# Kernel optimization log

Hardware: AMD Instinct MI355X
Metric: run time of the kernel (lower is better)

## Reference

```python
import jax, jax.numpy as jnp
import numpy as np


def _quat_to_rot(q):
    # q: (N,4) wxyz -> (N,3,3)
    q = q / jnp.linalg.norm(q, axis=1, keepdims=True)
    w, x, y, z = q[:, 0], q[:, 1], q[:, 2], q[:, 3]
    R = jnp.stack([
        1 - 2 * y * y - 2 * z * z, 2 * x * y - 2 * w * z, 2 * x * z + 2 * w * y,
        2 * x * y + 2 * w * z, 1 - 2 * x * x - 2 * z * z, 2 * y * z - 2 * w * x,
        2 * x * z - 2 * w * y, 2 * y * z + 2 * w * x, 1 - 2 * x * x - 2 * y * y,
    ], axis=1)
    return R.reshape(-1, 3, 3)


def _forward(camera_poses, positions, scales, rotations, opacity, features, H, W):
    B = camera_poses.shape[0]
    N = positions.shape[0]
    # --- project positions: hom @ pose^T ---
    hom = jnp.concatenate([positions, jnp.ones((N, 1), positions.dtype)], axis=1)  # (N,4)
    cam = jnp.einsum('ni,bji->bnj', hom, camera_poses)  # (B,N,4)
    depths = cam[..., 2]                                 # (B,N)
    pos2d = cam[..., :2] / depths[..., None]             # (B,N,2)
    # --- 3D covariance: R S S R^T ---
    R = _quat_to_rot(rotations)                          # (N,3,3)
    cov3d = jnp.einsum('nik,nk,njk->nij', R, scales * scales, R)  # (N,3,3)
    # --- perspective Jacobian (original uses world-space z, kept faithful) ---
    fx = camera_poses[:, 0, 0][:, None]  # (B,1)
    fy = camera_poses[:, 1, 1][:, None]
    z = positions[:, 2][None, :]         # (1,N)
    zero = jnp.zeros_like(fx * z)        # (B,N)
    row0 = jnp.stack([fx / z, zero, -fx * positions[None, :, 0] / (z * z)], axis=-1)
    row1 = jnp.stack([zero, fy / z, -fy * positions[None, :, 1] / (z * z)], axis=-1)
    J = jnp.stack([row0, row1], axis=-2)                 # (B,N,2,3)
    cov2d = jnp.einsum('bnij,njk,bnlk->bnil', J, cov3d, J)  # (B,N,2,2)
    # --- back-to-front order (descending depth) ---
    order = jnp.argsort(-depths, axis=1)                 # (B,N)
    pos_s = jnp.take_along_axis(pos2d, order[..., None], axis=1)
    cov_s = jnp.take_along_axis(cov2d, order[..., None, None], axis=1)
    color_s = features[order]                            # (B,N,3)
    alpha_s = opacity[order, 0]                          # (B,N)
    # analytic 2x2 inverse
    a = cov_s[..., 0, 0]; b = cov_s[..., 0, 1]; c = cov_s[..., 1, 0]; d = cov_s[..., 1, 1]
    det = a * d - b * c
    inv = jnp.stack([jnp.stack([d, -b], -1), jnp.stack([-c, a], -1)], -2) / det[..., None, None]
    # pixel grid in [-1,1], (H,W,2) with x first (matches torch stack([x,y]))
    ys = jnp.linspace(-1.0, 1.0, H)
    xs = jnp.linspace(-1.0, 1.0, W)
    yy, xx = jnp.meshgrid(ys, xs, indexing='ij')
    grid = jnp.stack([xx, yy], axis=-1)
    # --- splat + alpha compositing (sequential loop expressed as exclusive cumprod) ---
    diff = grid[None, None] - pos_s[:, :, None, None, :]           # (B,N,H,W,2)
    maha = jnp.einsum('bnhwi,bnij,bnhwj->bnhw', diff, inv, diff)   # (B,N,H,W)
    alpha_map = jnp.exp(-0.5 * maha) * alpha_s[:, :, None, None]   # (B,N,H,W)
    trans = jnp.cumprod(1.0 - alpha_map, axis=1)
    T = jnp.concatenate([jnp.ones_like(trans[:, :1]), trans[:, :-1]], axis=1)  # exclusive
    weight = T * alpha_map
    return jnp.einsum('bnhw,bnc->bchw', weight, color_s)          # (B,3,H,W)


def setup_inputs() -> dict:
    key = jax.random.key(0)
    ks = jax.random.split(key, 6)
    N, B = 2048, 1
    positions = jax.random.uniform(ks[0], (N, 3), minval=-1.0, maxval=1.0)
    scales = jax.random.uniform(ks[1], (N, 3), minval=0.001, maxval=0.1)
    rot = jnp.concatenate([jnp.ones((N, 1)), 0.01 * jax.random.normal(ks[2], (N, 3))], axis=1)
    rotations = rot / jnp.linalg.norm(rot, axis=1, keepdims=True)
    opacity = jax.random.uniform(ks[3], (N, 1), minval=0.0, maxval=0.02)
    features = jax.random.uniform(ks[4], (N, 3))
    pose = jnp.eye(4) + 0.01 * jax.random.normal(ks[5], (4, 4))
    pose = pose.at[2, 3].add(3.0).at[3].set(jnp.array([0.0, 0.0, 0.0, 1.0]))
    camera_poses = jnp.broadcast_to(pose, (B, 4, 4))
    return {"camera_poses": camera_poses, "positions": positions, "scales": scales,
            "rotations": rotations, "opacity": opacity, "features": features,
            "H": 96, "W": 96}


def reference(camera_poses, positions, scales, rotations, opacity, features, H, W):
    return _forward(camera_poses, positions, scales, rotations, opacity, features, H, W)
```

## Files before the change

kernel.cpp:

```cpp
#include <hip/hip_runtime.h>
#include <math.h>

#define TPB 256
#define PIXPT 4
#define NSEG_MAX 64

__device__ __forceinline__ unsigned int f2ord(float f) {
    unsigned int u = __float_as_uint(f);
    return (u & 0x80000000u) ? ~u : (u | 0x80000000u);
}

__global__ void gs_preprocess(const float* __restrict__ pose,
                              const float* __restrict__ positions,
                              const float* __restrict__ scales,
                              const float* __restrict__ rotations,
                              const float* __restrict__ opacity,
                              const float* __restrict__ features,
                              float* __restrict__ params,
                              unsigned long long* __restrict__ keys,
                              int N, int B)
{
    int idx = blockIdx.x * blockDim.x + threadIdx.x;
    if (idx >= B * N) return;
    int b = idx / N;
    int n = idx - b * N;
    const float* P = pose + b * 16;
    const float C_EXP = -0.72134752044448170f;

    float x = positions[n * 3 + 0];
    float y = positions[n * 3 + 1];
    float z = positions[n * 3 + 2];

    float depth = P[8] * x + P[9] * y + P[10] * z + P[11];
    float inv_d = 1.0f / depth;
    float mx = (P[0] * x + P[1] * y + P[2] * z + P[3]) * inv_d;
    float my = (P[4] * x + P[5] * y + P[6] * z + P[7]) * inv_d;

    float qw = rotations[n * 4 + 0];
    float qx = rotations[n * 4 + 1];
    float qy = rotations[n * 4 + 2];
    float qz = rotations[n * 4 + 3];
    float qn = sqrtf(qw * qw + qx * qx + qy * qy + qz * qz);
    qw /= qn; qx /= qn; qy /= qn; qz /= qn;
    float R00 = 1.f - 2.f * (qy * qy + qz * qz);
    float R01 = 2.f * (qx * qy - qw * qz);
    float R02 = 2.f * (qx * qz + qw * qy);
    float R10 = 2.f * (qx * qy + qw * qz);
    float R11 = 1.f - 2.f * (qx * qx + qz * qz);
    float R12 = 2.f * (qy * qz - qw * qx);
    float R20 = 2.f * (qx * qz - qw * qy);
    float R21 = 2.f * (qy * qz + qw * qx);
    float R22 = 1.f - 2.f * (qx * qx + qy * qy);

    float s0 = scales[n * 3 + 0];
    float s1 = scales[n * 3 + 1];
    float s2 = scales[n * 3 + 2];
    float v0 = s0 * s0, v1 = s1 * s1, v2 = s2 * s2;

    float C00 = R00 * R00 * v0 + R01 * R01 * v1 + R02 * R02 * v2;
    float C01 = R00 * R10 * v0 + R01 * R11 * v1 + R02 * R12 * v2;
    float C02 = R00 * R20 * v0 + R01 * R21 * v1 + R02 * R22 * v2;
    float C11 = R10 * R10 * v0 + R11 * R11 * v1 + R12 * R12 * v2;
    float C12 = R10 * R20 * v0 + R11 * R21 * v1 + R12 * R22 * v2;
    float C22 = R20 * R20 * v0 + R21 * R21 * v1 + R22 * R22 * v2;

    float fx = P[0], fy = P[5];
    float iz = 1.0f / z;
    float a0 = fx * iz;
    float c0 = -fx * x * iz * iz;
    float b1 = fy * iz;
    float c1 = -fy * y * iz * iz;

    float cov00 = a0 * a0 * C00 + 2.f * a0 * c0 * C02 + c0 * c0 * C22;
    float cov01 = a0 * b1 * C01 + a0 * c1 * C02 + c0 * b1 * C12 + c0 * c1 * C22;
    float cov11 = b1 * b1 * C11 + 2.f * b1 * c1 * C12 + c1 * c1 * C22;

    float det = cov00 * cov11 - cov01 * cov01;
    float invdet = 1.0f / det;
    float A  = C_EXP * cov11 * invdet;
    float Bc = C_EXP * -2.0f * cov01 * invdet;
    float D  = C_EXP * cov00 * invdet;
    float l2a = log2f(opacity[n]);

    float4* p4 = (float4*)(params + (size_t)idx * 12);
    p4[0] = make_float4(mx, my, A, Bc);
    p4[1] = make_float4(D, l2a, features[n * 3 + 0], features[n * 3 + 1]);
    p4[2] = make_float4(features[n * 3 + 2], 0.f, 0.f, 0.f);

    keys[idx] = ((unsigned long long)(~f2ord(depth)) << 32) | (unsigned int)n;
}

__global__ void gs_rank(const unsigned long long* __restrict__ keys,
                        int* __restrict__ order,
                        int N)
{
    extern __shared__ unsigned long long skey[];
    int b = blockIdx.y;
    const unsigned long long* kb = keys + (size_t)b * N;
    for (int i = threadIdx.x; i < N; i += blockDim.x) skey[i] = kb[i];
    __syncthreads();

    int g = blockIdx.x * 32 + (threadIdx.x >> 3);
    int s = threadIdx.x & 7;
    if (g >= N) return;
    unsigned long long kn = skey[g];
    int chunk = (N + 7) >> 3;
    int m0 = s * chunk;
    int m1 = m0 + chunk; if (m1 > N) m1 = N;
    int cnt = 0;
    #pragma unroll 4
    for (int m = m0; m < m1; ++m) cnt += (skey[m] < kn) ? 1 : 0;
    cnt += __shfl_down(cnt, 4, 8);
    cnt += __shfl_down(cnt, 2, 8);
    cnt += __shfl_down(cnt, 1, 8);
    if (s == 0) order[(size_t)b * N + cnt] = g;
}

__global__ void gs_raster_partial(const float* __restrict__ params,
                                  const int* __restrict__ order,
                                  float* __restrict__ partials,
                                  const int* __restrict__ pH,
                                  const int* __restrict__ pW,
                                  int N, int B, int HW, int nseg)
{
    extern __shared__ float4 sg4[];
    int H = *pH;
    int W = *pW;
    int seg = blockIdx.y;
    int seglen = (N + nseg - 1) / nseg;
    int g0 = seg * seglen;
    int g1 = g0 + seglen; if (g1 > N) g1 = N;
    int cnt = g1 - g0; if (cnt < 0) cnt = 0;

    int pixbase = blockIdx.x * (TPB * PIXPT);
    int b = pixbase / HW;

    const int* ob = order + (size_t)b * N + g0;
    for (int i = threadIdx.x; i < cnt * 3; i += TPB) {
        int gi = i / 3;
        int r  = i - gi * 3;
        int idx = ob[gi];
        sg4[i] = ((const float4*)(params + ((size_t)b * N + idx) * 12))[r];
    }
    __syncthreads();

    float px[PIXPT], py[PIXPT];
    float T[PIXPT], cr[PIXPT], cg[PIXPT], cb[PIXPT];
    bool valid[PIXPT];
    #pragma unroll
    for (int k = 0; k < PIXPT; ++k) {
        int pix = pixbase + threadIdx.x + k * TPB;
        valid[k] = (pix < B * HW);
        int pp = valid[k] ? (pix - b * HW) : 0;
        int h = pp / W;
        int w = pp - h * W;
        px[k] = 2.0f * (float)w / (float)(W - 1) - 1.0f;
        py[k] = 2.0f * (float)h / (float)(H - 1) - 1.0f;
        T[k] = 1.0f; cr[k] = 0.f; cg[k] = 0.f; cb[k] = 0.f;
    }

    for (int g = 0; g < cnt; ++g) {
        float4 f0 = sg4[g * 3 + 0];
        float4 f1 = sg4[g * 3 + 1];
        float4 f2 = sg4[g * 3 + 2];
        #pragma unroll
        for (int k = 0; k < PIXPT; ++k) {
            float dx = px[k] - f0.x;
            float dy = py[k] - f0.y;
            float q = f1.y;
            q = fmaf(f1.x * dy, dy, q);
            q = fmaf(f0.w * dx, dy, q);
            q = fmaf(f0.z * dx, dx, q);
            float am = exp2f(q);
            float wgt = T[k] * am;
            cr[k] = fmaf(wgt, f1.z, cr[k]);
            cg[k] = fmaf(wgt, f1.w, cg[k]);
            cb[k] = fmaf(wgt, f2.x, cb[k]);
            T[k] = fmaf(-am, T[k], T[k]);
        }
    }

    #pragma unroll
    for (int k = 0; k < PIXPT; ++k) {
        int pix = pixbase + threadIdx.x + k * TPB;
        if (!valid[k]) continue;
        float4* o = (float4*)(partials + ((size_t)seg * (size_t)(B * HW) + pix) * 4);
        *o = make_float4(cr[k], cg[k], cb[k], T[k]);
    }
}

__global__ void gs_combine(const float* __restrict__ partials,
                           float* __restrict__ out,
                           int B, int HW, int nseg)
{
    int pix = blockIdx.x * blockDim.x + threadIdx.x;
    if (pix >= B * HW) return;
    int b = pix / HW;
    int pp = pix - b * HW;
    float T = 1.0f, cr = 0.f, cg = 0.f, cb = 0.f;
    for (int s = 0; s < nseg; ++s) {
        float4 p = *(const float4*)(partials + ((size_t)s * (size_t)(B * HW) + pix) * 4);
        cr = fmaf(T, p.x, cr);
        cg = fmaf(T, p.y, cg);
        cb = fmaf(T, p.z, cb);
        T *= p.w;
    }
    out[((size_t)b * 3 + 0) * HW + pp] = cr;
    out[((size_t)b * 3 + 1) * HW + pp] = cg;
    out[((size_t)b * 3 + 2) * HW + pp] = cb;
}

extern "C" void kernel_launch(void* const* d_in, const int* in_sizes, int n_in,
                              void* d_out, int out_size, void* d_ws, size_t ws_size,
                              hipStream_t stream)
{
    const float* pose      = (const float*)d_in[0];
    const float* positions = (const float*)d_in[1];
    const float* scales    = (const float*)d_in[2];
    const float* rotations = (const float*)d_in[3];
    const float* opacity   = (const float*)d_in[4];
    const float* features  = (const float*)d_in[5];
    const int*   pH        = (const int*)d_in[6];
    const int*   pW        = (const int*)d_in[7];

    int B = in_sizes[0] / 16;
    int N = in_sizes[1] / 3;
    int HW = out_size / (3 * B);

    float* out = (float*)d_out;

    char* wp = (char*)d_ws;
    float* params = (float*)wp;
    wp += ((size_t)B * N * 12 * sizeof(float) + 15) & ~(size_t)15;
    unsigned long long* keys = (unsigned long long*)wp;
    wp += ((size_t)B * N * sizeof(unsigned long long) + 15) & ~(size_t)15;
    int* order = (int*)wp;
    wp += ((size_t)B * N * sizeof(int) + 15) & ~(size_t)15;
    float* partials = (float*)wp;

    size_t used = (size_t)(wp - (char*)d_ws);
    size_t avail = ws_size > used ? ws_size - used : 0;
    long long ns = (long long)(avail / ((size_t)B * HW * 4 * sizeof(float)));
    int nseg = (int)(ns > NSEG_MAX ? NSEG_MAX : ns);
    if (nseg < 1) nseg = 1;

    int bn = B * N;
    gs_preprocess<<<(bn + TPB - 1) / TPB, TPB, 0, stream>>>(
        pose, positions, scales, rotations, opacity, features,
        params, keys, N, B);

    dim3 g2((N + 31) / 32, B);
    gs_rank<<<g2, TPB, N * sizeof(unsigned long long), stream>>>(keys, order, N);

    int seglen = (N + nseg - 1) / nseg;
    dim3 g3((B * HW + TPB * PIXPT - 1) / (TPB * PIXPT), nseg);
    gs_raster_partial<<<g3, TPB, (size_t)seglen * 3 * sizeof(float4), stream>>>(
        params, order, partials, pH, pW, N, B, HW, nseg);

    gs_combine<<<(B * HW + TPB - 1) / TPB, TPB, 0, stream>>>(
        partials, out, B, HW, nseg);
}
```

Before: 124.3 us.

## Fuse preprocess and rank kernels, scatter params directly in sorted order

Merges the preprocessing and rank-counting kernels into one launch. Each block recomputes all depth keys into shared memory, ranks its Gaussians, and the rank-0 lane of each group computes the full parameters and writes them straight to their sorted slot. The raster kernel then reads the sorted parameter array contiguously instead of gathering through an order index. This removes one launch, the keys and order buffers, and the indirect gather. In exchange, every block recomputes all N depths, and the per-Gaussian math runs on only one lane in eight, which is divergent. The rank loop now uses a strided access pattern instead of contiguous chunks.

Result: faster. 120.9 us (-2.8%).

```diff
diff --git a/kernel.cpp b/kernel.cpp
--- a/kernel.cpp
+++ b/kernel.cpp
@@ -10,36 +10,54 @@
     return (u & 0x80000000u) ? ~u : (u | 0x80000000u);
 }
 
-__global__ void gs_preprocess(const float* __restrict__ pose,
-                              const float* __restrict__ positions,
-                              const float* __restrict__ scales,
-                              const float* __restrict__ rotations,
-                              const float* __restrict__ opacity,
-                              const float* __restrict__ features,
-                              float* __restrict__ params,
-                              unsigned long long* __restrict__ keys,
-                              int N, int B)
-{
-    int idx = blockIdx.x * blockDim.x + threadIdx.x;
-    if (idx >= B * N) return;
-    int b = idx / N;
-    int n = idx - b * N;
+__global__ void gs_prep_rank(const float* __restrict__ pose,
+                             const float* __restrict__ positions,
+                             const float* __restrict__ scales,
+                             const float* __restrict__ rotations,
+                             const float* __restrict__ opacity,
+                             const float* __restrict__ features,
+                             float* __restrict__ sorted,
+                             int N)
+{
+    extern __shared__ unsigned long long skey[];
+    const int b = blockIdx.y;
     const float* P = pose + b * 16;
     const float C_EXP = -0.72134752044448170f;
 
-    float x = positions[n * 3 + 0];
-    float y = positions[n * 3 + 1];
-    float z = positions[n * 3 + 2];
+    for (int n = threadIdx.x; n < N; n += TPB) {
+        float x = positions[n * 3 + 0];
+        float y = positions[n * 3 + 1];
+        float z = positions[n * 3 + 2];
+        float depth = P[8] * x + P[9] * y + P[10] * z + P[11];
+        skey[n] = ((unsigned long long)(~f2ord(depth)) << 32) | (unsigned int)n;
+    }
+    __syncthreads();
+
+    int g = blockIdx.x * 32 + (threadIdx.x >> 3);
+    int s = threadIdx.x & 7;
+    if (g >= N) return;
+    unsigned long long kn = skey[g];
+    int cnt = 0;
+    for (int m = s; m < N; m += 8) cnt += (skey[m] < kn) ? 1 : 0;
+    cnt += __shfl_down(cnt, 4, 8);
+    cnt += __shfl_down(cnt, 2, 8);
+    cnt += __shfl_down(cnt, 1, 8);
+    if (s != 0) return;
+    int rank = cnt;
+
+    float x = positions[g * 3 + 0];
+    float y = positions[g * 3 + 1];
+    float z = positions[g * 3 + 2];
 
     float depth = P[8] * x + P[9] * y + P[10] * z + P[11];
     float inv_d = 1.0f / depth;
     float mx = (P[0] * x + P[1] * y + P[2] * z + P[3]) * inv_d;
     float my = (P[4] * x + P[5] * y + P[6] * z + P[7]) * inv_d;
 
-    float qw = rotations[n * 4 + 0];
-    float qx = rotations[n * 4 + 1];
-    float qy = rotations[n * 4 + 2];
-    float qz = rotations[n * 4 + 3];
+    float qw = rotations[g * 4 + 0];
+    float qx = rotations[g * 4 + 1];
+    float qy = rotations[g * 4 + 2];
+    float qz = rotations[g * 4 + 3];
     float qn = sqrtf(qw * qw + qx * qx + qy * qy + qz * qz);
     qw /= qn; qx /= qn; qy /= qn; qz /= qn;
     float R00 = 1.f - 2.f * (qy * qy + qz * qz);
@@ -52,9 +70,9 @@
     float R21 = 2.f * (qy * qz + qw * qx);
     float R22 = 1.f - 2.f * (qx * qx + qy * qy);
 
-    float s0 = scales[n * 3 + 0];
-    float s1 = scales[n * 3 + 1];
-    float s2 = scales[n * 3 + 2];
+    float s0 = scales[g * 3 + 0];
+    float s1 = scales[g * 3 + 1];
+    float s2 = scales[g * 3 + 2];
     float v0 = s0 * s0, v1 = s1 * s1, v2 = s2 * s2;
 
     float C00 = R00 * R00 * v0 + R01 * R01 * v1 + R02 * R02 * v2;
@@ -80,44 +98,15 @@
     float A  = C_EXP * cov11 * invdet;
     float Bc = C_EXP * -2.0f * cov01 * invdet;
     float D  = C_EXP * cov00 * invdet;
-    float l2a = log2f(opacity[n]);
-
-    float4* p4 = (float4*)(params + (size_t)idx * 12);
+    float l2a = log2f(opacity[g]);
+
+    float4* p4 = (float4*)(sorted + ((size_t)b * N + rank) * 12);
     p4[0] = make_float4(mx, my, A, Bc);
-    p4[1] = make_float4(D, l2a, features[n * 3 + 0], features[n * 3 + 1]);
-    p4[2] = make_float4(features[n * 3 + 2], 0.f, 0.f, 0.f);
-
-    keys[idx] = ((unsigned long long)(~f2ord(depth)) << 32) | (unsigned int)n;
-}
-
-__global__ void gs_rank(const unsigned long long* __restrict__ keys,
-                        int* __restrict__ order,
-                        int N)
-{
-    extern __shared__ unsigned long long skey[];
-    int b = blockIdx.y;
-    const unsigned long long* kb = keys + (size_t)b * N;
-    for (int i = threadIdx.x; i < N; i += blockDim.x) skey[i] = kb[i];
-    __syncthreads();
-
-    int g = blockIdx.x * 32 + (threadIdx.x >> 3);
-    int s = threadIdx.x & 7;
-    if (g >= N) return;
-    unsigned long long kn = skey[g];
-    int chunk = (N + 7) >> 3;
-    int m0 = s * chunk;
-    int m1 = m0 + chunk; if (m1 > N) m1 = N;
-    int cnt = 0;
-    #pragma unroll 4
-    for (int m = m0; m < m1; ++m) cnt += (skey[m] < kn) ? 1 : 0;
-    cnt += __shfl_down(cnt, 4, 8);
-    cnt += __shfl_down(cnt, 2, 8);
-    cnt += __shfl_down(cnt, 1, 8);
-    if (s == 0) order[(size_t)b * N + cnt] = g;
-}
-
-__global__ void gs_raster_partial(const float* __restrict__ params,
-                                  const int* __restrict__ order,
+    p4[1] = make_float4(D, l2a, features[g * 3 + 0], features[g * 3 + 1]);
+    p4[2] = make_float4(features[g * 3 + 2], 0.f, 0.f, 0.f);
+}
+
+__global__ void gs_raster_partial(const float* __restrict__ sorted,
                                   float* __restrict__ partials,
                                   const int* __restrict__ pH,
                                   const int* __restrict__ pW,
@@ -135,13 +124,8 @@
     int pixbase = blockIdx.x * (TPB * PIXPT);
     int b = pixbase / HW;
 
-    const int* ob = order + (size_t)b * N + g0;
-    for (int i = threadIdx.x; i < cnt * 3; i += TPB) {
-        int gi = i / 3;
-        int r  = i - gi * 3;
-        int idx = ob[gi];
-        sg4[i] = ((const float4*)(params + ((size_t)b * N + idx) * 12))[r];
-    }
+    const float4* src = (const float4*)(sorted + ((size_t)b * N + g0) * 12);
+    for (int i = threadIdx.x; i < cnt * 3; i += TPB) sg4[i] = src[i];
     __syncthreads();
 
     float px[PIXPT], py[PIXPT];
@@ -230,12 +214,8 @@
     float* out = (float*)d_out;
 
     char* wp = (char*)d_ws;
-    float* params = (float*)wp;
+    float* sorted = (float*)wp;
     wp += ((size_t)B * N * 12 * sizeof(float) + 15) & ~(size_t)15;
-    unsigned long long* keys = (unsigned long long*)wp;
-    wp += ((size_t)B * N * sizeof(unsigned long long) + 15) & ~(size_t)15;
-    int* order = (int*)wp;
-    wp += ((size_t)B * N * sizeof(int) + 15) & ~(size_t)15;
     float* partials = (float*)wp;
 
     size_t used = (size_t)(wp - (char*)d_ws);
@@ -244,18 +224,14 @@
     int nseg = (int)(ns > NSEG_MAX ? NSEG_MAX : ns);
     if (nseg < 1) nseg = 1;
 
-    int bn = B * N;
-    gs_preprocess<<<(bn + TPB - 1) / TPB, TPB, 0, stream>>>(
-        pose, positions, scales, rotations, opacity, features,
-        params, keys, N, B);
-
-    dim3 g2((N + 31) / 32, B);
-    gs_rank<<<g2, TPB, N * sizeof(unsigned long long), stream>>>(keys, order, N);
+    dim3 g1((N + 31) / 32, B);
+    gs_prep_rank<<<g1, TPB, N * sizeof(unsigned long long), stream>>>(
+        pose, positions, scales, rotations, opacity, features, sorted, N);
 
     int seglen = (N + nseg - 1) / nseg;
     dim3 g3((B * HW + TPB * PIXPT - 1) / (TPB * PIXPT), nseg);
     gs_raster_partial<<<g3, TPB, (size_t)seglen * 3 * sizeof(float4), stream>>>(
-        params, order, partials, pH, pW, N, B, HW, nseg);
+        sorted, partials, pH, pW, N, B, HW, nseg);
 
     gs_combine<<<(B * HW + TPB - 1) / TPB, TPB, 0, stream>>>(
         partials, out, B, HW, nseg);
```
